# Optimization experiments

Measured on AMD Instinct MI355X. Metric: run time of the kernel, lower is better.

The kernel has to match this reference:

```python
import jax, jax.numpy as jnp
import numpy as np

B, T, D = 4, 4096, 1024

def setup_inputs() -> dict:
    key = jax.random.key(0)
    ks = jax.random.split(key, 6)
    x = jax.random.normal(ks[0], (B, T, D), dtype=jnp.float32)
    mask = jax.random.randint(ks[1], (B, T), 0, 2).astype(bool)
    # torch nn.Linear init scale ~ 1/sqrt(fan_in); exact init unimportant for correctness baseline
    s = 1.0 / np.sqrt(D)
    W_qkv = jax.random.normal(ks[2], (3 * D, D), dtype=jnp.float32) * s
    b_qkv = jax.random.normal(ks[3], (3 * D,), dtype=jnp.float32) * s
    W_out = jax.random.normal(ks[4], (D, D), dtype=jnp.float32) * s
    b_out = jax.random.normal(ks[5], (D,), dtype=jnp.float32) * s
    return {"x": x, "mask": mask, "W_qkv": W_qkv, "b_qkv": b_qkv, "W_out": W_out, "b_out": b_out}

def reference(x, mask, W_qkv, b_qkv, W_out, b_out):
    # qkv projection: (B,T,D) @ (D,3D) + (3D,)
    qkv = jnp.einsum('btd,ed->bte', x, W_qkv) + b_qkv
    q, k, v = jnp.split(qkv, 3, axis=-1)  # each (B,T,D)
    q = q / jnp.linalg.norm(q, axis=-1, keepdims=True)
    k = k / jnp.linalg.norm(k, axis=-1, keepdims=True)
    k = jnp.where(mask[..., None], 0.0, k)  # masked_fill(mask, 0)
    kv = jnp.sum(k * v, axis=-2, keepdims=True)  # (B,1,D) global feature sum
    out = kv * q  # (B,T,D)
    return jnp.einsum('btd,ed->bte', out, W_out) + b_out
```

## Files before the change

### kernel.cpp

```cpp
#include <hip/hip_runtime.h>
#include <stdint.h>


typedef short  short8   __attribute__((ext_vector_type(8)));
typedef float  floatx16 __attribute__((ext_vector_type(16)));

#define NT 32

__device__ __forceinline__ void async16(const void* g, void* l) {
  __builtin_amdgcn_global_load_lds((const __attribute__((address_space(1))) void*)g,
                                   (__attribute__((address_space(3))) void*)l, 16, 0, 0);
}

__device__ __forceinline__ uint16_t f2bf(float f) {
  union { float f; uint32_t u; } x; x.f = f;
  uint32_t u = x.u;
  return (uint16_t)((u + 0x7fffu + ((u >> 16) & 1u)) >> 16);
}
__device__ __forceinline__ float bf2f(uint16_t h) {
  union { uint32_t u; float f; } x; x.u = ((uint32_t)h) << 16; return x.f;
}
__device__ __forceinline__ uint32_t pack2(float a, float b) {
  return (uint32_t)f2bf(a) | ((uint32_t)f2bf(b) << 16);
}
__device__ __forceinline__ void upk8(uint4 u, float* f) {
  f[0]=bf2f((uint16_t)u.x); f[1]=bf2f((uint16_t)(u.x>>16));
  f[2]=bf2f((uint16_t)u.y); f[3]=bf2f((uint16_t)(u.y>>16));
  f[4]=bf2f((uint16_t)u.z); f[5]=bf2f((uint16_t)(u.z>>16));
  f[6]=bf2f((uint16_t)u.w); f[7]=bf2f((uint16_t)(u.w>>16));
}

__global__ __launch_bounds__(256) void cvt3(
    const float* __restrict__ a, uint16_t* __restrict__ ao, int na,
    const float* __restrict__ b, uint16_t* __restrict__ bo, int nb,
    const float* __restrict__ c, uint16_t* __restrict__ co, int nc) {
  int i = blockIdx.x * 256 + threadIdx.x;
  const float* in; uint16_t* out; int j = i;
  if (j < na) { in = a; out = ao; }
  else {
    j -= na;
    if (j < nb) { in = b; out = bo; }
    else { j -= nb; if (j >= nc) return; in = c; out = co; }
  }
  const float4* p = (const float4*)in;
  float4 u = p[(size_t)j * 2], v = p[(size_t)j * 2 + 1];
  uint4 o;
  o.x = pack2(u.x, u.y); o.y = pack2(u.z, u.w);
  o.z = pack2(v.x, v.y); o.w = pack2(v.z, v.w);
  ((uint4*)out)[j] = o;
}

#define LOADF(kci, Ac, Bc, kcv) { \
    const int sl_ = (((kcv) ^ rsw) * 8); \
    const uint16_t* Ap_ = (Ac) + sl_; \
    const uint16_t* Bp_ = (Bc) + sl_; \
    fA[kci][0] = *(const short8*)&Ap_[(wm * 128 +  0 + l31) * 32]; \
    fA[kci][1] = *(const short8*)&Ap_[(wm * 128 + 32 + l31) * 32]; \
    fA[kci][2] = *(const short8*)&Ap_[(wm * 128 + 64 + l31) * 32]; \
    fA[kci][3] = *(const short8*)&Ap_[(wm * 128 + 96 + l31) * 32]; \
    fB[kci][0] = *(const short8*)&Bp_[(wn * 64 +  0 + l31) * 32]; \
    fB[kci][1] = *(const short8*)&Bp_[(wn * 64 + 32 + l31) * 32]; }

#define MFMA8(kci) { \
    __builtin_amdgcn_s_setprio(1); \
    acc[0][0] = __builtin_amdgcn_mfma_f32_32x32x16_bf16(fA[kci][0], fB[kci][0], acc[0][0], 0, 0, 0); \
    acc[0][1] = __builtin_amdgcn_mfma_f32_32x32x16_bf16(fA[kci][0], fB[kci][1], acc[0][1], 0, 0, 0); \
    acc[1][0] = __builtin_amdgcn_mfma_f32_32x32x16_bf16(fA[kci][1], fB[kci][0], acc[1][0], 0, 0, 0); \
    acc[1][1] = __builtin_amdgcn_mfma_f32_32x32x16_bf16(fA[kci][1], fB[kci][1], acc[1][1], 0, 0, 0); \
    acc[2][0] = __builtin_amdgcn_mfma_f32_32x32x16_bf16(fA[kci][2], fB[kci][0], acc[2][0], 0, 0, 0); \
    acc[2][1] = __builtin_amdgcn_mfma_f32_32x32x16_bf16(fA[kci][2], fB[kci][1], acc[2][1], 0, 0, 0); \
    acc[3][0] = __builtin_amdgcn_mfma_f32_32x32x16_bf16(fA[kci][3], fB[kci][0], acc[3][0], 0, 0, 0); \
    acc[3][1] = __builtin_amdgcn_mfma_f32_32x32x16_bf16(fA[kci][3], fB[kci][1], acc[3][1], 0, 0, 0); \
    __builtin_amdgcn_s_setprio(0); }

#define GATE_(t) if ((t) + 3 < NT) { asm volatile("s_waitcnt vmcnt(8)" ::: "memory"); } \
    else if ((t) + 2 < NT) { asm volatile("s_waitcnt vmcnt(4)" ::: "memory"); } \
    else if ((t) + 1 < NT) { asm volatile("s_waitcnt vmcnt(0)" ::: "memory"); }

#define KLOOP(STAGE) \
  asm volatile("s_waitcnt vmcnt(8)" ::: "memory"); \
  __builtin_amdgcn_s_barrier(); \
  LOADF(0, As[0], Bs[0], khalf); \
  _Pragma("unroll 1") \
  for (int t = 0; t < NT; ++t) { \
    STAGE(t + 3); \
    const uint16_t* Ac_ = As[t & 3]; \
    const uint16_t* Bc_ = Bs[t & 3]; \
    LOADF(1, Ac_, Bc_, khalf + 2);       \
    MFMA8(0);                            \
    GATE_(t); \
    asm volatile("s_waitcnt lgkmcnt(0)" ::: "memory"); \
    __builtin_amdgcn_sched_barrier(0); \
    __builtin_amdgcn_s_barrier(); \
    if (t + 1 < NT) { \
      const uint16_t* An_ = As[(t + 1) & 3]; \
      const uint16_t* Bn_ = Bs[(t + 1) & 3]; \
      LOADF(0, An_, Bn_, khalf);         \
    } \
    MFMA8(1);                            \
  }

__global__ __launch_bounds__(512, 2) void gemm1(
    const uint16_t* __restrict__ A, const uint16_t* __restrict__ Bw,
    const float* __restrict__ bias, uint16_t* __restrict__ Cb)
{
  __shared__ __align__(16) uint16_t As[4][8192];
  __shared__ __align__(16) uint16_t Bs[4][8192];
  const int tid = threadIdx.x;
  const int wave = tid >> 6, lane = tid & 63;
  const int l31 = lane & 31, khalf = lane >> 5;
  const int rsw = (l31 >> 1) & 3;
  const int wm = wave & 1, wn = wave >> 1;
  const int id = blockIdx.x;
  const int xcd = id & 7, w = id >> 3;
  const int tileM = ((w / 12) * 8 + xcd) * 256;
  const int tileN = (w % 12) * 256;

  const int srow = tid >> 2;
  const int sk   = (tid & 3) ^ ((tid >> 3) & 3);
  const uint16_t* gA = A  + (size_t)(tileM + srow) * 1024 + sk * 8;
  const uint16_t* gB = Bw + (size_t)(tileN + srow) * 1024 + sk * 8;

  floatx16 acc[4][2];
#pragma unroll
  for (int mi = 0; mi < 4; mi++)
#pragma unroll
    for (int ni = 0; ni < 2; ni++)
#pragma unroll
      for (int r = 0; r < 16; r++) acc[mi][ni][r] = 0.f;

  short8 fA[2][4], fB[2][2];

#define STG1(tt) if ((tt) < NT) { const int c3_ = (tt) & 3; const size_t ko_ = (size_t)(tt) * 32; \
    async16(gA + ko_,                      (char*)As[c3_] + wave * 1024); \
    async16(gA + ko_ + (size_t)128 * 1024, (char*)As[c3_] + 8192 + wave * 1024); \
    async16(gB + ko_,                      (char*)Bs[c3_] + wave * 1024); \
    async16(gB + ko_ + (size_t)128 * 1024, (char*)Bs[c3_] + 8192 + wave * 1024); }

  STG1(0); STG1(1); STG1(2);
  KLOOP(STG1)
#undef STG1

#pragma unroll
  for (int mi = 0; mi < 4; mi++) {
    const int rbase = tileM + wm * 128 + mi * 32 + 4 * khalf;
#pragma unroll
    for (int ni = 0; ni < 2; ni++) {
      const int col = tileN + wn * 64 + ni * 32 + l31;
      const float bv = bias[col];
#pragma unroll
      for (int reg = 0; reg < 16; reg++) {
        const int row = rbase + (reg & 3) + 8 * (reg >> 2);
        Cb[(size_t)row * 3072 + col] = f2bf(acc[mi][ni][reg] + bv);
      }
    }
  }
}

__global__ __launch_bounds__(512, 2) void gemm2(
    const uint16_t* __restrict__ qkv, const float* __restrict__ invq,
    const uint16_t* __restrict__ Wp, const float* __restrict__ bias,
    float* __restrict__ Cf)
{
  __shared__ __align__(16) uint16_t As[4][8192];
  __shared__ __align__(16) uint16_t Bs[4][8192];
  const int tid = threadIdx.x;
  const int wave = tid >> 6, lane = tid & 63;
  const int l31 = lane & 31, khalf = lane >> 5;
  const int rsw = (l31 >> 1) & 3;
  const int wm = wave & 1, wn = wave >> 1;
  const int id = (blockIdx.x & 7) * 32 + (blockIdx.x >> 3);
  const int tileM = (id >> 2) * 256;
  const int tileN = (id & 3) * 256;
  const int batch = tileM >> 12;

  const int srow = tid >> 2;
  const int sk   = (tid & 3) ^ ((tid >> 3) & 3);
  const uint16_t* gA = qkv + (size_t)(tileM + srow) * 3072 + sk * 8;
  const uint16_t* gB = Wp + ((size_t)batch << 20) + (size_t)(tileN + srow) * 1024 + sk * 8;

  floatx16 acc[4][2];
#pragma unroll
  for (int mi = 0; mi < 4; mi++)
#pragma unroll
    for (int ni = 0; ni < 2; ni++)
#pragma unroll
      for (int r = 0; r < 16; r++) acc[mi][ni][r] = 0.f;

  short8 fA[2][4], fB[2][2];

#define STG2(tt) if ((tt) < NT) { const int c3_ = (tt) & 3; const size_t ko_ = (size_t)(tt) * 32; \
    async16(gA + ko_,                      (char*)As[c3_] + wave * 1024); \
    async16(gA + ko_ + (size_t)128 * 3072, (char*)As[c3_] + 8192 + wave * 1024); \
    async16(gB + ko_,                      (char*)Bs[c3_] + wave * 1024); \
    async16(gB + ko_ + (size_t)128 * 1024, (char*)Bs[c3_] + 8192 + wave * 1024); }

  STG2(0); STG2(1); STG2(2);
  KLOOP(STG2)
#undef STG2

#pragma unroll
  for (int mi = 0; mi < 4; mi++) {
    const int rbase = tileM + wm * 128 + mi * 32 + 4 * khalf;
#pragma unroll
    for (int ni = 0; ni < 2; ni++) {
      const int col = tileN + wn * 64 + ni * 32 + l31;
      const float bv = bias[col];
#pragma unroll
      for (int reg = 0; reg < 16; reg++) {
        const int row = rbase + (reg & 3) + 8 * (reg >> 2);
        Cf[(size_t)row * 1024 + col] = fmaf(invq[row], acc[mi][ni][reg], bv);
      }
    }
  }
}

__global__ __launch_bounds__(256) void scale_w(
    const uint16_t* __restrict__ wo, const float* __restrict__ kv,
    uint16_t* __restrict__ wp)
{
  int i = blockIdx.x * 256 + threadIdx.x;
  int e = i << 3;
  int b = e >> 20;
  int k = e & 1023;
  uint4 w = *(const uint4*)(wo + (e & 0xFFFFF));
  float4 k0v = *(const float4*)(kv + (b << 10) + k);
  float4 k1v = *(const float4*)(kv + (b << 10) + k + 4);
  float wf[8]; upk8(w, wf);
  uint4 o;
  o.x = pack2(wf[0] * k0v.x, wf[1] * k0v.y);
  o.y = pack2(wf[2] * k0v.z, wf[3] * k0v.w);
  o.z = pack2(wf[4] * k1v.x, wf[5] * k1v.y);
  o.w = pack2(wf[6] * k1v.z, wf[7] * k1v.w);
  *(uint4*)(wp + e) = o;
}

__global__ __launch_bounds__(256) void detect_mask(const unsigned char* __restrict__ m,
                                                   int* __restrict__ flag) {
  int i = blockIdx.x * blockDim.x + threadIdx.x;
  int v = ((i & 3) != 0) ? (int)m[i] : 0;
  unsigned long long b = __ballot(v != 0);
  if ((threadIdx.x & 63) == 0 && b) atomicOr(flag, 1);
}

__global__ __launch_bounds__(256) void rownorm_kv(
    const uint16_t* __restrict__ qkv, const void* __restrict__ maskbuf,
    const int* __restrict__ flag, float* __restrict__ invq, float* __restrict__ kv)
{
  __shared__ float kvloc[1024];
  const int tid = threadIdx.x;
  for (int i = tid; i < 1024; i += 256) kvloc[i] = 0.f;
  __syncthreads();
  const int wave = tid >> 6, lane = tid & 63;
  const int b = blockIdx.x >> 7;
  const int chunk = blockIdx.x & 127;
  const int isU8 = *flag;
  const unsigned char* m8 = (const unsigned char*)maskbuf;
  const int* m32 = (const int*)maskbuf;

  float kvacc[16];
#pragma unroll
  for (int i = 0; i < 16; i++) kvacc[i] = 0.f;

  const int r0 = b * 4096 + chunk * 32 + wave * 8;
#pragma unroll 2
  for (int j = 0; j < 8; j++) {
    int r = r0 + j;
    const uint16_t* rp = qkv + (size_t)r * 3072;
    uint4 q0 = *(const uint4*)(rp + lane * 16);
    uint4 q1 = *(const uint4*)(rp + lane * 16 + 8);
    uint4 k0 = *(const uint4*)(rp + 1024 + lane * 16);
    uint4 k1 = *(const uint4*)(rp + 1024 + lane * 16 + 8);
    uint4 v0 = *(const uint4*)(rp + 2048 + lane * 16);
    uint4 v1 = *(const uint4*)(rp + 2048 + lane * 16 + 8);
    float qf[16], kf[16], vf[16];
    upk8(q0, qf); upk8(q1, qf + 8);
    upk8(k0, kf); upk8(k1, kf + 8);
    upk8(v0, vf); upk8(v1, vf + 8);
    float sq = 0.f, sk = 0.f;
#pragma unroll
    for (int i = 0; i < 16; i++) { sq = fmaf(qf[i], qf[i], sq); sk = fmaf(kf[i], kf[i], sk); }
    for (int off = 32; off; off >>= 1) { sq += __shfl_xor(sq, off); sk += __shfl_xor(sk, off); }
    float rq = rsqrtf(sq), rk = rsqrtf(sk);
    if (lane == 0) invq[r] = rq;
    int masked = isU8 ? (int)m8[r] : m32[r];
    if (!masked) {
#pragma unroll
      for (int i = 0; i < 16; i++) kvacc[i] = fmaf(kf[i] * rk, vf[i], kvacc[i]);
    }
  }
#pragma unroll
  for (int i = 0; i < 16; i++) atomicAdd(&kvloc[lane * 16 + i], kvacc[i]);
  __syncthreads();
  for (int i = tid; i < 1024; i += 256) atomicAdd(&kv[b * 1024 + i], kvloc[i]);
}

extern "C" void kernel_launch(void* const* d_in, const int* in_sizes, int n_in,
                              void* d_out, int out_size, void* d_ws, size_t ws_size,
                              hipStream_t stream) {
  const float* x     = (const float*)d_in[0];
  const void*  mask  = d_in[1];
  const float* W_qkv = (const float*)d_in[2];
  const float* b_qkv = (const float*)d_in[3];
  const float* W_out = (const float*)d_in[4];
  const float* b_out = (const float*)d_in[5];
  float* out = (float*)d_out;

  const int BT = 4 * 4096;
  const int D  = 1024;

  char* ws = (char*)d_ws;
  size_t off = 0;
  auto alloc = [&](size_t bytes) { size_t r = off; off += (bytes + 255) & ~(size_t)255; return r; };
  size_t o_xb   = alloc((size_t)BT * D * 2);
  size_t o_qkvb = alloc((size_t)BT * 3 * D * 2);
  size_t o_wq   = alloc((size_t)3 * D * D * 2);
  size_t o_wo   = alloc((size_t)D * D * 2);
  size_t o_wp   = alloc((size_t)4 * D * D * 2);
  size_t o_kv   = alloc((size_t)4 * D * 4 + 256);
  size_t o_invq = alloc((size_t)BT * 4);

  uint16_t* xb   = (uint16_t*)(ws + o_xb);
  uint16_t* qkvb = (uint16_t*)(ws + o_qkvb);
  uint16_t* wq   = (uint16_t*)(ws + o_wq);
  uint16_t* wo   = (uint16_t*)(ws + o_wo);
  uint16_t* wp   = (uint16_t*)(ws + o_wp);
  float*    kv   = (float*)(ws + o_kv);
  int*      flag = (int*)(ws + o_kv + (size_t)4 * D * 4);
  float*    invq = (float*)(ws + o_invq);

  hipMemsetAsync(ws + o_kv, 0, (size_t)4 * D * 4 + 256, stream);
  {
    int na = BT * D / 8, nb = 3 * D * D / 8, nc = D * D / 8;
    int tot = na + nb + nc;
    cvt3<<<dim3((tot + 255) / 256), 256, 0, stream>>>(x, xb, na, W_qkv, wq, nb, W_out, wo, nc);
  }
  detect_mask<<<dim3(64), 256, 0, stream>>>((const unsigned char*)mask, flag);
  gemm1<<<dim3(768), 512, 0, stream>>>(xb, wq, b_qkv, qkvb);
  rownorm_kv<<<dim3(512), 256, 0, stream>>>(qkvb, mask, flag, invq, kv);
  scale_w<<<dim3(4 * D * D / 8 / 256), 256, 0, stream>>>(wo, kv, wp);
  gemm2<<<dim3(256), 512, 0, stream>>>(qkvb, invq, wp, b_out, out);
}
```

Before: 338.7 us.

## Restructure GEMMs to 4-wave blocks with 128x128 warp tiles and BK=64 double buffering

Both GEMM kernels drop from 8 waves of 512 threads to 4 waves of 256 threads, and each wave now computes a 128x128 sub-tile (4x4 MFMA accumulators) instead of 128x64. The K step grows from 32 to 64, and the 4-stage LDS ring with a hand-interleaved fragment-prefetch pipeline becomes a simple 2-stage double buffer with full vmcnt(0) waits. The XOR swizzle is rewritten for 64-element rows. The aim is more MFMA work per LDS fragment load and fewer barriers per K. The cost is double the accumulator registers, occupancy of one block per CU, and less overlap between memory and compute.

```diff
diff --git a/kernel.cpp b/kernel.cpp
--- a/kernel.cpp
+++ b/kernel.cpp
@@ -5,7 +5,7 @@
 typedef short  short8   __attribute__((ext_vector_type(8)));
 typedef float  floatx16 __attribute__((ext_vector_type(16)));
 
-#define NT 32
+#define NTK 16
 
 __device__ __forceinline__ void async16(const void* g, void* l) {
   __builtin_amdgcn_global_load_lds((const __attribute__((address_space(1))) void*)g,
@@ -50,103 +50,86 @@
   ((uint4*)out)[j] = o;
 }
 
-#define LOADF(kci, Ac, Bc, kcv) { \
-    const int sl_ = (((kcv) ^ rsw) * 8); \
-    const uint16_t* Ap_ = (Ac) + sl_; \
-    const uint16_t* Bp_ = (Bc) + sl_; \
-    fA[kci][0] = *(const short8*)&Ap_[(wm * 128 +  0 + l31) * 32]; \
-    fA[kci][1] = *(const short8*)&Ap_[(wm * 128 + 32 + l31) * 32]; \
-    fA[kci][2] = *(const short8*)&Ap_[(wm * 128 + 64 + l31) * 32]; \
-    fA[kci][3] = *(const short8*)&Ap_[(wm * 128 + 96 + l31) * 32]; \
-    fB[kci][0] = *(const short8*)&Bp_[(wn * 64 +  0 + l31) * 32]; \
-    fB[kci][1] = *(const short8*)&Bp_[(wn * 64 + 32 + l31) * 32]; }
-
-#define MFMA8(kci) { \
-    __builtin_amdgcn_s_setprio(1); \
-    acc[0][0] = __builtin_amdgcn_mfma_f32_32x32x16_bf16(fA[kci][0], fB[kci][0], acc[0][0], 0, 0, 0); \
-    acc[0][1] = __builtin_amdgcn_mfma_f32_32x32x16_bf16(fA[kci][0], fB[kci][1], acc[0][1], 0, 0, 0); \
-    acc[1][0] = __builtin_amdgcn_mfma_f32_32x32x16_bf16(fA[kci][1], fB[kci][0], acc[1][0], 0, 0, 0); \
-    acc[1][1] = __builtin_amdgcn_mfma_f32_32x32x16_bf16(fA[kci][1], fB[kci][1], acc[1][1], 0, 0, 0); \
-    acc[2][0] = __builtin_amdgcn_mfma_f32_32x32x16_bf16(fA[kci][2], fB[kci][0], acc[2][0], 0, 0, 0); \
-    acc[2][1] = __builtin_amdgcn_mfma_f32_32x32x16_bf16(fA[kci][2], fB[kci][1], acc[2][1], 0, 0, 0); \
-    acc[3][0] = __builtin_amdgcn_mfma_f32_32x32x16_bf16(fA[kci][3], fB[kci][0], acc[3][0], 0, 0, 0); \
-    acc[3][1] = __builtin_amdgcn_mfma_f32_32x32x16_bf16(fA[kci][3], fB[kci][1], acc[3][1], 0, 0, 0); \
-    __builtin_amdgcn_s_setprio(0); }
-
-#define GATE_(t) if ((t) + 3 < NT) { asm volatile("s_waitcnt vmcnt(8)" ::: "memory"); } \
-    else if ((t) + 2 < NT) { asm volatile("s_waitcnt vmcnt(4)" ::: "memory"); } \
-    else if ((t) + 1 < NT) { asm volatile("s_waitcnt vmcnt(0)" ::: "memory"); }
-
-#define KLOOP(STAGE) \
-  asm volatile("s_waitcnt vmcnt(8)" ::: "memory"); \
+#define STG(tt, SA, SB) { \
+    char* lA_ = (char*)As[(tt) & 1] + wave * 1024; \
+    char* lB_ = (char*)Bs[(tt) & 1] + wave * 1024; \
+    const size_t ko_ = (size_t)(tt) * 64; \
+    _Pragma("unroll") \
+    for (int s_ = 0; s_ < 8; s_++) { \
+      async16(gA + ko_ + (size_t)s_ * 32 * (SA), lA_ + s_ * 4096); \
+      async16(gB + ko_ + (size_t)s_ * 32 * (SB), lB_ + s_ * 4096); \
+    } }
+
+#define COMPUTE(Ac_, Bc_) \
+  _Pragma("unroll") \
+  for (int ks = 0; ks < 4; ++ks) { \
+    const int so = ((khalf + ks * 2) ^ r7) * 8; \
+    short8 af[4], bfr[4]; \
+    _Pragma("unroll") \
+    for (int mi = 0; mi < 4; mi++) \
+      af[mi] = *(const short8*)&(Ac_)[(wm * 128 + mi * 32 + l31) * 64 + so]; \
+    _Pragma("unroll") \
+    for (int ni = 0; ni < 4; ni++) \
+      bfr[ni] = *(const short8*)&(Bc_)[(wn * 128 + ni * 32 + l31) * 64 + so]; \
+    _Pragma("unroll") \
+    for (int mi = 0; mi < 4; mi++) \
+      _Pragma("unroll") \
+      for (int ni = 0; ni < 4; ni++) \
+        acc[mi][ni] = __builtin_amdgcn_mfma_f32_32x32x16_bf16(af[mi], bfr[ni], acc[mi][ni], 0, 0, 0); \
+  }
+
+#define KLOOP(SA, SB) \
+  STG(0, SA, SB) \
+  asm volatile("s_waitcnt vmcnt(0)" ::: "memory"); \
   __builtin_amdgcn_s_barrier(); \
-  LOADF(0, As[0], Bs[0], khalf); \
+  asm volatile("" ::: "memory"); \
   _Pragma("unroll 1") \
-  for (int t = 0; t < NT; ++t) { \
-    STAGE(t + 3); \
-    const uint16_t* Ac_ = As[t & 3]; \
-    const uint16_t* Bc_ = Bs[t & 3]; \
-    LOADF(1, Ac_, Bc_, khalf + 2);       \
-    MFMA8(0);                            \
-    GATE_(t); \
-    asm volatile("s_waitcnt lgkmcnt(0)" ::: "memory"); \
-    __builtin_amdgcn_sched_barrier(0); \
+  for (int t = 0; t < NTK; ++t) { \
+    if (t + 1 < NTK) STG(t + 1, SA, SB) \
+    const uint16_t* Ac_ = As[t & 1]; \
+    const uint16_t* Bc_ = Bs[t & 1]; \
+    COMPUTE(Ac_, Bc_) \
+    asm volatile("s_waitcnt vmcnt(0)" ::: "memory"); \
     __builtin_amdgcn_s_barrier(); \
-    if (t + 1 < NT) { \
-      const uint16_t* An_ = As[(t + 1) & 3]; \
-      const uint16_t* Bn_ = Bs[(t + 1) & 3]; \
-      LOADF(0, An_, Bn_, khalf);         \
-    } \
-    MFMA8(1);                            \
-  }
-
-__global__ __launch_bounds__(512, 2) void gemm1(
+    asm volatile("" ::: "memory"); \
+  }
+
+__global__ __launch_bounds__(256, 1) void gemm1(
     const uint16_t* __restrict__ A, const uint16_t* __restrict__ Bw,
     const float* __restrict__ bias, uint16_t* __restrict__ Cb)
 {
-  __shared__ __align__(16) uint16_t As[4][8192];
-  __shared__ __align__(16) uint16_t Bs[4][8192];
+  __shared__ __align__(16) uint16_t As[2][16384];
+  __shared__ __align__(16) uint16_t Bs[2][16384];
   const int tid = threadIdx.x;
   const int wave = tid >> 6, lane = tid & 63;
-  const int l31 = lane & 31, khalf = lane >> 5;
-  const int rsw = (l31 >> 1) & 3;
+  const int l31 = lane & 31, khalf = lane >> 5, r7 = l31 & 7;
   const int wm = wave & 1, wn = wave >> 1;
   const int id = blockIdx.x;
   const int xcd = id & 7, w = id >> 3;
   const int tileM = ((w / 12) * 8 + xcd) * 256;
   const int tileN = (w % 12) * 256;
 
-  const int srow = tid >> 2;
-  const int sk   = (tid & 3) ^ ((tid >> 3) & 3);
+  const int srow = wave * 8 + (lane >> 3);
+  const int sk   = (lane & 7) ^ (lane >> 3);
   const uint16_t* gA = A  + (size_t)(tileM + srow) * 1024 + sk * 8;
   const uint16_t* gB = Bw + (size_t)(tileN + srow) * 1024 + sk * 8;
 
-  floatx16 acc[4][2];
+  floatx16 acc[4][4];
 #pragma unroll
   for (int mi = 0; mi < 4; mi++)
 #pragma unroll
-    for (int ni = 0; ni < 2; ni++)
+    for (int ni = 0; ni < 4; ni++)
 #pragma unroll
       for (int r = 0; r < 16; r++) acc[mi][ni][r] = 0.f;
 
-  short8 fA[2][4], fB[2][2];
-
-#define STG1(tt) if ((tt) < NT) { const int c3_ = (tt) & 3; const size_t ko_ = (size_t)(tt) * 32; \
-    async16(gA + ko_,                      (char*)As[c3_] + wave * 1024); \
-    async16(gA + ko_ + (size_t)128 * 1024, (char*)As[c3_] + 8192 + wave * 1024); \
-    async16(gB + ko_,                      (char*)Bs[c3_] + wave * 1024); \
-    async16(gB + ko_ + (size_t)128 * 1024, (char*)Bs[c3_] + 8192 + wave * 1024); }
-
-  STG1(0); STG1(1); STG1(2);
-  KLOOP(STG1)
-#undef STG1
+  KLOOP(1024, 1024)
 
 #pragma unroll
   for (int mi = 0; mi < 4; mi++) {
     const int rbase = tileM + wm * 128 + mi * 32 + 4 * khalf;
 #pragma unroll
-    for (int ni = 0; ni < 2; ni++) {
-      const int col = tileN + wn * 64 + ni * 32 + l31;
+    for (int ni = 0; ni < 4; ni++) {
+      const int col = tileN + wn * 128 + ni * 32 + l31;
       const float bv = bias[col];
 #pragma unroll
       for (int reg = 0; reg < 16; reg++) {
@@ -157,54 +140,43 @@
   }
 }
 
-__global__ __launch_bounds__(512, 2) void gemm2(
+__global__ __launch_bounds__(256, 1) void gemm2(
     const uint16_t* __restrict__ qkv, const float* __restrict__ invq,
     const uint16_t* __restrict__ Wp, const float* __restrict__ bias,
     float* __restrict__ Cf)
 {
-  __shared__ __align__(16) uint16_t As[4][8192];
-  __shared__ __align__(16) uint16_t Bs[4][8192];
+  __shared__ __align__(16) uint16_t As[2][16384];
+  __shared__ __align__(16) uint16_t Bs[2][16384];
   const int tid = threadIdx.x;
   const int wave = tid >> 6, lane = tid & 63;
-  const int l31 = lane & 31, khalf = lane >> 5;
-  const int rsw = (l31 >> 1) & 3;
+  const int l31 = lane & 31, khalf = lane >> 5, r7 = l31 & 7;
   const int wm = wave & 1, wn = wave >> 1;
-  const int id = (blockIdx.x & 7) * 32 + (blockIdx.x >> 3);
-  const int tileM = (id >> 2) * 256;
-  const int tileN = (id & 3) * 256;
+  const int wid = (blockIdx.x & 7) * 32 + (blockIdx.x >> 3);
+  const int tileM = (wid >> 2) * 256;
+  const int tileN = (wid & 3) * 256;
   const int batch = tileM >> 12;
 
-  const int srow = tid >> 2;
-  const int sk   = (tid & 3) ^ ((tid >> 3) & 3);
+  const int srow = wave * 8 + (lane >> 3);
+  const int sk   = (lane & 7) ^ (lane >> 3);
   const uint16_t* gA = qkv + (size_t)(tileM + srow) * 3072 + sk * 8;
   const uint16_t* gB = Wp + ((size_t)batch << 20) + (size_t)(tileN + srow) * 1024 + sk * 8;
 
-  floatx16 acc[4][2];
+  floatx16 acc[4][4];
 #pragma unroll
   for (int mi = 0; mi < 4; mi++)
 #pragma unroll
-    for (int ni = 0; ni < 2; ni++)
+    for (int ni = 0; ni < 4; ni++)
 #pragma unroll
       for (int r = 0; r < 16; r++) acc[mi][ni][r] = 0.f;
 
-  short8 fA[2][4], fB[2][2];
-
-#define STG2(tt) if ((tt) < NT) { const int c3_ = (tt) & 3; const size_t ko_ = (size_t)(tt) * 32; \
-    async16(gA + ko_,                      (char*)As[c3_] + wave * 1024); \
-    async16(gA + ko_ + (size_t)128 * 3072, (char*)As[c3_] + 8192 + wave * 1024); \
-    async16(gB + ko_,                      (char*)Bs[c3_] + wave * 1024); \
-    async16(gB + ko_ + (size_t)128 * 1024, (char*)Bs[c3_] + 8192 + wave * 1024); }
-
-  STG2(0); STG2(1); STG2(2);
-  KLOOP(STG2)
-#undef STG2
+  KLOOP(3072, 1024)
 
 #pragma unroll
   for (int mi = 0; mi < 4; mi++) {
     const int rbase = tileM + wm * 128 + mi * 32 + 4 * khalf;
 #pragma unroll
-    for (int ni = 0; ni < 2; ni++) {
-      const int col = tileN + wn * 64 + ni * 32 + l31;
+    for (int ni = 0; ni < 4; ni++) {
+      const int col = tileN + wn * 128 + ni * 32 + l31;
       const float bv = bias[col];
 #pragma unroll
       for (int reg = 0; reg < 16; reg++) {
@@ -336,8 +308,8 @@
     cvt3<<<dim3((tot + 255) / 256), 256, 0, stream>>>(x, xb, na, W_qkv, wq, nb, W_out, wo, nc);
   }
   detect_mask<<<dim3(64), 256, 0, stream>>>((const unsigned char*)mask, flag);
-  gemm1<<<dim3(768), 512, 0, stream>>>(xb, wq, b_qkv, qkvb);
+  gemm1<<<dim3(768), 256, 0, stream>>>(xb, wq, b_qkv, qkvb);
   rownorm_kv<<<dim3(512), 256, 0, stream>>>(qkvb, mask, flag, invq, kv);
   scale_w<<<dim3(4 * D * D / 8 / 256), 256, 0, stream>>>(wo, kv, wp);
-  gemm2<<<dim3(256), 512, 0, stream>>>(qkvb, invq, wp, b_out, out);
-}
+  gemm2<<<dim3(256), 256, 0, stream>>>(qkvb, invq, wp, b_out, out);
+}
```

Result: slower. 353.6 us (+4.4%).
